# Optimization experiments

Hardware: AMD Instinct MI355X
Metric: run time of the kernel (lower is better)

Reference implementation:

```python
import jax, jax.numpy as jnp
import numpy as np

POOL = 7  # pool_size


def setup_inputs() -> dict:
    key = jax.random.key(0)
    k1, k2, k3, k4, k5 = jax.random.split(key, 5)
    H = W = 64
    C = 1024
    R = 1024  # num_rois
    img = jax.random.normal(k1, (1, H, W, C), dtype=jnp.float32)
    x = jax.random.randint(k2, (1, R), 0, W - 16)
    y = jax.random.randint(k3, (1, R), 0, H - 16)
    w = jax.random.randint(k4, (1, R), 1, 17)
    h = jax.random.randint(k5, (1, R), 1, 17)
    rois = jnp.stack([x, y, w, h], axis=-1).astype(jnp.int32)  # (1, R, 4)
    return {"img": img, "rois": rois}


def _axis_coords(start, size, pool):
    """Per-ROI bilinear source coords for tf.image.resize (half-pixel centers).
    start,size: (R,) int32. Returns absolute low/high indices (R,pool) int32
    and interpolation weight (R,pool) float32."""
    scale = size.astype(jnp.float32) / pool
    src = (jnp.arange(pool, dtype=jnp.float32) + 0.5)[None, :] * scale[:, None] - 0.5
    f = jnp.floor(src)
    lerp = src - f
    lo = jnp.clip(f.astype(jnp.int32), 0, size[:, None] - 1)
    hi = jnp.clip(f.astype(jnp.int32) + 1, 0, size[:, None] - 1)
    return start[:, None] + lo, start[:, None] + hi, lerp


def reference(img, rois):
    # img: (1, H, W, C); rois: (1, R, 4) int32 with (x, y, w, h)
    r = rois[0]
    x, y, w, h = r[:, 0], r[:, 1], r[:, 2], r[:, 3]
    y0, y1, ty = _axis_coords(y, h, POOL)  # (R, P)
    x0, x1, tx = _axis_coords(x, w, POOL)  # (R, P)
    im = img[0]  # (H, W, C)

    def gather(yy, xx):
        # (R, P, P, C) corner gather, vectorized over all ROIs
        return im[yy[:, :, None], xx[:, None, :], :]

    tx_ = tx[:, None, :, None]
    ty_ = ty[:, :, None, None]
    top = gather(y0, x0) * (1.0 - tx_) + gather(y0, x1) * tx_
    bot = gather(y1, x0) * (1.0 - tx_) + gather(y1, x1) * tx_
    out = top * (1.0 - ty_) + bot * ty_  # (R, P, P, C)
    return out[None]  # (1, R, P, P, C)
```

## Files before the change

### kernel.cpp

```cpp
#include <hip/hip_runtime.h>


#define POOLSZ 7
#define IMG_H 64
#define IMG_W 64
#define IMG_C 1024
#define NUM_XCD 8

typedef float v4f __attribute__((ext_vector_type(4)));

__global__ __launch_bounds__(256) void roi_pool_kernel(
    const float* __restrict__ img,
    const int* __restrict__ rois,
    float* __restrict__ out,
    int roisPerXcd) {
    int r, cell;
    if (roisPerXcd > 0) {
        const int xcd   = blockIdx.x & (NUM_XCD - 1);
        const int local = blockIdx.x >> 3;
        r    = xcd * roisPerXcd + local / (POOLSZ * POOLSZ);
        cell = local % (POOLSZ * POOLSZ);
    } else {
        r    = blockIdx.x / (POOLSZ * POOLSZ);
        cell = blockIdx.x % (POOLSZ * POOLSZ);
    }
    const int px = cell % POOLSZ;
    const int py = cell / POOLSZ;

    const int4 roi = ((const int4*)rois)[r];
    const int rx = roi.x, ry = roi.y, rw = roi.z, rh = roi.w;

    const float scy  = (float)rh * (1.0f / (float)POOLSZ);
    const float srcy = ((float)py + 0.5f) * scy - 0.5f;
    const float fy   = floorf(srcy);
    const float ty   = srcy - fy;
    const int   iy   = (int)fy;
    const int   y0   = ry + min(max(iy,     0), rh - 1);
    const int   y1   = ry + min(max(iy + 1, 0), rh - 1);

    const float scx  = (float)rw * (1.0f / (float)POOLSZ);
    const float srcx = ((float)px + 0.5f) * scx - 0.5f;
    const float fx   = floorf(srcx);
    const float tx   = srcx - fx;
    const int   ix   = (int)fx;
    const int   x0   = rx + min(max(ix,     0), rw - 1);
    const int   x1   = rx + min(max(ix + 1, 0), rw - 1);

    const int c4 = threadIdx.x;

    const v4f* p00 = (const v4f*)(img + ((size_t)y0 * IMG_W + x0) * IMG_C) + c4;
    const v4f* p01 = (const v4f*)(img + ((size_t)y0 * IMG_W + x1) * IMG_C) + c4;
    const v4f* p10 = (const v4f*)(img + ((size_t)y1 * IMG_W + x0) * IMG_C) + c4;
    const v4f* p11 = (const v4f*)(img + ((size_t)y1 * IMG_W + x1) * IMG_C) + c4;

    const v4f a = *p00;
    const v4f b = *p01;
    const v4f c = *p10;
    const v4f d = *p11;

    const v4f top = a + (b - a) * tx;
    const v4f bot = c + (d - c) * tx;
    const v4f o   = top + (bot - top) * ty;

    v4f* dst = (v4f*)out + ((size_t)r * (POOLSZ * POOLSZ) + cell) * (IMG_C / 4) + c4;
    __builtin_nontemporal_store(o, dst);
}

extern "C" void kernel_launch(void* const* d_in, const int* in_sizes, int n_in,
                              void* d_out, int out_size, void* d_ws, size_t ws_size,
                              hipStream_t stream) {
    const float* img  = (const float*)d_in[0];
    const int*   rois = (const int*)d_in[1];
    float*       out  = (float*)d_out;
    const int R = in_sizes[1] / 4;
    const int n_cells = R * POOLSZ * POOLSZ;
    const int roisPerXcd = (R % NUM_XCD == 0) ? (R / NUM_XCD) : 0;
    roi_pool_kernel<<<n_cells, 256, 0, stream>>>(img, rois, out, roisPerXcd);
}
```

Baseline: 241.2 us.

## Stage ROI patch per channel group in LDS via async global-to-LDS loads

Each block now handles one ROI and one 64-channel group. It first copies the whole ROI pixel patch (up to 16x16) for that group into shared memory using global_load_lds direct transfers, then computes all 49 bilinear cells from LDS. The aim is to replace four redundant global corner gathers per output cell with a single patch load reused across cells. The cost is that every pixel in the ROI is loaded, even pixels no sample uses, plus a block-wide barrier and 64KB of LDS per block, which limits occupancy. The XCD-aware block remapping is removed.

Result: slower. 248.3 us (+3.0%).

```diff
diff --git a/kernel.cpp b/kernel.cpp
--- a/kernel.cpp
+++ b/kernel.cpp
@@ -2,68 +2,105 @@
 
 
 #define POOLSZ 7
-#define IMG_H 64
 #define IMG_W 64
 #define IMG_C 1024
-#define NUM_XCD 8
+#define GROUP 64
+#define NQUAD (GROUP / 4)
+#define NGROUP (IMG_C / GROUP)
+#define MAXPX 256
 
 typedef float v4f __attribute__((ext_vector_type(4)));
+typedef __attribute__((address_space(1))) const void as1_cvoid;
+typedef __attribute__((address_space(3))) void as3_void;
 
-__global__ __launch_bounds__(256) void roi_pool_kernel(
+__global__ __launch_bounds__(256, 2) void roi_pool_lds_kernel(
     const float* __restrict__ img,
     const int* __restrict__ rois,
-    float* __restrict__ out,
-    int roisPerXcd) {
-    int r, cell;
-    if (roisPerXcd > 0) {
-        const int xcd   = blockIdx.x & (NUM_XCD - 1);
-        const int local = blockIdx.x >> 3;
-        r    = xcd * roisPerXcd + local / (POOLSZ * POOLSZ);
-        cell = local % (POOLSZ * POOLSZ);
-    } else {
-        r    = blockIdx.x / (POOLSZ * POOLSZ);
-        cell = blockIdx.x % (POOLSZ * POOLSZ);
-    }
-    const int px = cell % POOLSZ;
-    const int py = cell / POOLSZ;
+    float* __restrict__ out) {
+
+    __shared__ v4f smem[MAXPX * NQUAD];
+
+    const int bid = blockIdx.x;
+    const int g   = bid & (NGROUP - 1);
+    const int r   = bid >> 4;
 
     const int4 roi = ((const int4*)rois)[r];
     const int rx = roi.x, ry = roi.y, rw = roi.z, rh = roi.w;
+    const int npx   = rw * rh;
+    const int total = npx * NQUAD;
 
-    const float scy  = (float)rh * (1.0f / (float)POOLSZ);
-    const float srcy = ((float)py + 0.5f) * scy - 0.5f;
-    const float fy   = floorf(srcy);
-    const float ty   = srcy - fy;
-    const int   iy   = (int)fy;
-    const int   y0   = ry + min(max(iy,     0), rh - 1);
-    const int   y1   = ry + min(max(iy + 1, 0), rh - 1);
+    const unsigned magic = (65536u + (unsigned)rw - 1u) / (unsigned)rw;
 
-    const float scx  = (float)rw * (1.0f / (float)POOLSZ);
-    const float srcx = ((float)px + 0.5f) * scx - 0.5f;
-    const float fx   = floorf(srcx);
-    const float tx   = srcx - fx;
-    const int   ix   = (int)fx;
-    const int   x0   = rx + min(max(ix,     0), rw - 1);
-    const int   x1   = rx + min(max(ix + 1, 0), rw - 1);
+    const float* src0 = img + ((size_t)ry * IMG_W + rx) * IMG_C + g * GROUP;
 
-    const int c4 = threadIdx.x;
+    const int tid  = threadIdx.x;
+    const int wave = tid >> 6;
 
-    const v4f* p00 = (const v4f*)(img + ((size_t)y0 * IMG_W + x0) * IMG_C) + c4;
-    const v4f* p01 = (const v4f*)(img + ((size_t)y0 * IMG_W + x1) * IMG_C) + c4;
-    const v4f* p10 = (const v4f*)(img + ((size_t)y1 * IMG_W + x0) * IMG_C) + c4;
-    const v4f* p11 = (const v4f*)(img + ((size_t)y1 * IMG_W + x1) * IMG_C) + c4;
+    const int nfull = total & ~255;
+    for (int base = 0; base < nfull; base += 256) {
+        const int idx = base + tid;
+        const int p   = idx >> 4;
+        const int q   = idx & 15;
+        const int py  = (int)(((unsigned)p * magic) >> 16);
+        const int px  = p - py * rw;
+        const float* src = src0 + ((size_t)((py << 6) + px)) * IMG_C + (q << 2);
+        __builtin_amdgcn_global_load_lds(
+            (as1_cvoid*)src,
+            (as3_void*)&smem[base + (wave << 6)],
+            16, 0, 0);
+    }
+    for (int idx = nfull + tid; idx < total; idx += 256) {
+        const int p  = idx >> 4;
+        const int q  = idx & 15;
+        const int py = (int)(((unsigned)p * magic) >> 16);
+        const int px = p - py * rw;
+        smem[idx] = ((const v4f*)(src0 + ((size_t)((py << 6) + px)) * IMG_C))[q];
+    }
+    __builtin_amdgcn_s_waitcnt(0);
+    __syncthreads();
 
-    const v4f a = *p00;
-    const v4f b = *p01;
-    const v4f c = *p10;
-    const v4f d = *p11;
+    const int q    = tid & 15;
+    const int slot = tid >> 4;
 
-    const v4f top = a + (b - a) * tx;
-    const v4f bot = c + (d - c) * tx;
-    const v4f o   = top + (bot - top) * ty;
+    const float inv7 = 1.0f / 7.0f;
+    const float scx  = (float)rw * inv7;
+    const float scy  = (float)rh * inv7;
 
-    v4f* dst = (v4f*)out + ((size_t)r * (POOLSZ * POOLSZ) + cell) * (IMG_C / 4) + c4;
-    __builtin_nontemporal_store(o, dst);
+    v4f* out4 = (v4f*)out + (size_t)r * (POOLSZ * POOLSZ) * (IMG_C / 4)
+                + g * NQUAD + q;
+
+#pragma unroll
+    for (int it = 0; it < 4; ++it) {
+        const int cell = it * 16 + slot;
+        if (cell < POOLSZ * POOLSZ) {
+            const int cy = cell / POOLSZ;
+            const int cx = cell - cy * POOLSZ;
+
+            const float srcy = ((float)cy + 0.5f) * scy - 0.5f;
+            const float fy   = floorf(srcy);
+            const float ty   = srcy - fy;
+            const int   iy   = (int)fy;
+            const int   y0   = min(max(iy,     0), rh - 1);
+            const int   y1   = min(max(iy + 1, 0), rh - 1);
+
+            const float srcx = ((float)cx + 0.5f) * scx - 0.5f;
+            const float fx   = floorf(srcx);
+            const float tx   = srcx - fx;
+            const int   ix   = (int)fx;
+            const int   x0   = min(max(ix,     0), rw - 1);
+            const int   x1   = min(max(ix + 1, 0), rw - 1);
+
+            const v4f a = smem[(y0 * rw + x0) * NQUAD + q];
+            const v4f b = smem[(y0 * rw + x1) * NQUAD + q];
+            const v4f c = smem[(y1 * rw + x0) * NQUAD + q];
+            const v4f d = smem[(y1 * rw + x1) * NQUAD + q];
+
+            const v4f top = a + (b - a) * tx;
+            const v4f bot = c + (d - c) * tx;
+            const v4f o   = top + (bot - top) * ty;
+            __builtin_nontemporal_store(o, out4 + (size_t)cell * (IMG_C / 4));
+        }
+    }
 }
 
 extern "C" void kernel_launch(void* const* d_in, const int* in_sizes, int n_in,
@@ -73,7 +110,6 @@
     const int*   rois = (const int*)d_in[1];
     float*       out  = (float*)d_out;
     const int R = in_sizes[1] / 4;
-    const int n_cells = R * POOLSZ * POOLSZ;
-    const int roisPerXcd = (R % NUM_XCD == 0) ? (R / NUM_XCD) : 0;
-    roi_pool_kernel<<<n_cells, 256, 0, stream>>>(img, rois, out, roisPerXcd);
+    const int n_blocks = R * NGROUP;
+    roi_pool_lds_kernel<<<n_blocks, 256, 0, stream>>>(img, rois, out);
 }
```
